# Optimization experiments

Hardware: AMD Instinct MI355X
Metric: run time of the kernel (lower is better)

Reference implementation:

```python
import jax, jax.numpy as jnp
import numpy as np

B, D, C = 512, 512, 100000
U_M, L_M, U_A, L_A = 0.8, 0.45, 110.0, 10.0
LAMBDA_G, SCALE = 35.0, 64.0


def setup_inputs() -> dict:
    key = jax.random.key(0)
    k1, k2, k3, k4 = jax.random.split(key, 4)
    x = jax.random.normal(k1, (B, D), dtype=jnp.float32)
    # magnitudes in [l_a, u_a] as in MagFace
    x_norm = L_A + (U_A - L_A) * jax.random.uniform(k2, (B,), dtype=jnp.float32)
    labels = jax.random.randint(k3, (B,), 0, C, dtype=jnp.int64)
    weight = jax.random.normal(k4, (C, D), dtype=jnp.float32)
    return {"x": x, "x_norm": x_norm, "labels": labels, "weight": weight}


def _l2norm(a, axis=-1, eps=1e-12):
    return a / jnp.maximum(jnp.linalg.norm(a, axis=axis, keepdims=True), eps)


def reference(x, x_norm, labels, weight):
    # adaptive margin per sample, shape [B]
    margin = (U_M - L_M) / (U_A - L_A) * (x_norm - L_A) + L_M

    # cos_theta = normalize(x) @ normalize(W).T  -> [B, C]
    cos_theta = jnp.clip(_l2norm(x) @ _l2norm(weight).T, -1.0, 1.0)

    theta = jnp.arccos(cos_theta)
    valid = labels != -1  # [B]
    safe_labels = jnp.where(valid, labels, 0)
    # add margin at the target class (only for valid labels)
    add = jnp.where(valid, margin, 0.0)  # [B]
    theta = theta.at[jnp.arange(theta.shape[0]), safe_labels].add(add)

    logits = jnp.cos(theta) * SCALE  # [B, C]

    # cross-entropy, ignoring labels == -1
    lse = jax.nn.logsumexp(logits, axis=-1)  # [B]
    tgt = jnp.take_along_axis(logits, safe_labels[:, None], axis=-1)[:, 0]
    nll = jnp.where(valid, lse - tgt, 0.0)
    n_valid = jnp.maximum(jnp.sum(valid.astype(jnp.float32)), 1.0)
    ce = jnp.sum(nll) / n_valid

    # MagFace G-loss
    g_loss = jnp.mean(x_norm / (U_A * U_A) + 1.0 / x_norm)

    return ce + LAMBDA_G * g_loss
```

## Files before the change

kernel.cpp:

```cpp
#include <hip/hip_runtime.h>

typedef unsigned short u16;
typedef unsigned int u32;
typedef float f32x4 __attribute__((ext_vector_type(4)));
typedef short bf16x8 __attribute__((ext_vector_type(8)));

#define U_M 0.8f
#define L_M 0.45f
#define U_A 110.0f
#define L_A 10.0f
#define LAMBDA_G 35.0f
#define SCALEF 64.0f

__device__ __forceinline__ u16 f2bf(float f) {
  u32 u = __builtin_bit_cast(u32, f);
  u32 r = (u + 0x7fffu + ((u >> 16) & 1u)) >> 16;
  return (u16)r;
}

__device__ __forceinline__ u32 cvtpk(float lo, float hi) {
  u32 r;
  asm("v_cvt_pk_bf16_f32 %0, %1, %2" : "=v"(r) : "v"(lo), "v"(hi));
  return r;
}

__global__ void xnorm_kernel(const float* __restrict__ x, u16* __restrict__ xn, int K) {
  int row = blockIdx.x * 4 + (threadIdx.x >> 6);
  int l = threadIdx.x & 63;
  const float4* p = reinterpret_cast<const float4*>(x + (size_t)row * K) + l * 2;
  float4 a = p[0], b = p[1];
  float s = a.x*a.x + a.y*a.y + a.z*a.z + a.w*a.w
          + b.x*b.x + b.y*b.y + b.z*b.z + b.w*b.w;
  #pragma unroll
  for (int m = 32; m >= 1; m >>= 1) s += __shfl_xor(s, m);
  float inv = rsqrtf(fmaxf(s, 1e-24f));
  u32 q0 = (u32)f2bf(a.x*inv) | ((u32)f2bf(a.y*inv) << 16);
  u32 q1 = (u32)f2bf(a.z*inv) | ((u32)f2bf(a.w*inv) << 16);
  u32 q2 = (u32)f2bf(b.x*inv) | ((u32)f2bf(b.y*inv) << 16);
  u32 q3 = (u32)f2bf(b.z*inv) | ((u32)f2bf(b.w*inv) << 16);
  *reinterpret_cast<uint4*>(xn + (size_t)row * K + l * 8) = make_uint4(q0, q1, q2, q3);
}

__global__ void tgt_kernel(const float* __restrict__ x, const float* __restrict__ W,
                           const int* __restrict__ labels, float* __restrict__ tgtcos, int K) {
  int b = blockIdx.x;
  int l = threadIdx.x;
  int lab = labels[b];
  int labc = lab < 0 ? 0 : lab;
  const float4* px = reinterpret_cast<const float4*>(x + (size_t)b * K) + l * 2;
  const float4* pw = reinterpret_cast<const float4*>(W + (size_t)labc * K) + l * 2;
  float4 a0 = px[0], a1 = px[1], w0 = pw[0], w1 = pw[1];
  float dot = a0.x*w0.x + a0.y*w0.y + a0.z*w0.z + a0.w*w0.w
            + a1.x*w1.x + a1.y*w1.y + a1.z*w1.z + a1.w*w1.w;
  float sx = a0.x*a0.x + a0.y*a0.y + a0.z*a0.z + a0.w*a0.w
           + a1.x*a1.x + a1.y*a1.y + a1.z*a1.z + a1.w*a1.w;
  float sw = w0.x*w0.x + w0.y*w0.y + w0.z*w0.z + w0.w*w0.w
           + w1.x*w1.x + w1.y*w1.y + w1.z*w1.z + w1.w*w1.w;
  #pragma unroll
  for (int m = 32; m >= 1; m >>= 1) {
    dot += __shfl_xor(dot, m);
    sx  += __shfl_xor(sx, m);
    sw  += __shfl_xor(sw, m);
  }
  if (l == 0) {
    float cv = dot * rsqrtf(fmaxf(sx, 1e-24f)) * rsqrtf(fmaxf(sw, 1e-24f));
    tgtcos[b] = fminf(fmaxf(cv, -1.f), 1.f);
  }
}

__global__ __launch_bounds__(512, 4) void gemm_wf32(
    const u16* __restrict__ xn, const float* __restrict__ W,
    const int* __restrict__ labels,
    float* __restrict__ partials, int C, int K, int M) {
  __shared__ u16 sA[2][128 * 64];
  __shared__ u16 sB[128 * 64];
  __shared__ float bsum[4][128];
  __shared__ float sIw[128];
  __shared__ int slab[128];

  int nwg = gridDim.x;
  int id = blockIdx.x;
  int q = nwg >> 3, r = nwg & 7;
  int xcd = id & 7, pos = id >> 3;
  int wg = (xcd < r ? xcd * (q + 1) : r * (q + 1) + (xcd - r) * q) + pos;
  const int bm = wg & 3, bn = wg >> 2;

  const int t = threadIdx.x;
  const int l = t & 63, wid = t >> 6;
  const int wm = wid >> 2, wn_ = wid & 3;
  const int n0 = bn * 128;
  if (t < 128) slab[t] = labels[bm * 128 + t];

  const int c4 = t & 15;
  const int rowL = t >> 4;
  const float* wp[4];
  #pragma unroll
  for (int p = 0; p < 4; ++p) {
    int rr = n0 + p * 32 + rowL;
    rr = rr < C ? rr : C - 1;
    wp[p] = W + (size_t)rr * K + c4 * 4;
  }
  float ssq[4] = {0.f, 0.f, 0.f, 0.f};

  const int nkt = K >> 6;
  float4 v[4];

  #pragma unroll
  for (int p = 0; p < 4; ++p) v[p] = *reinterpret_cast<const float4*>(wp[p]);
  #pragma unroll
  for (int i = 0; i < 2; ++i) {
    int L = i * 512 + t;
    int rr = L >> 3;
    int cs = (L & 7) ^ (rr & 7);
    const u16* src = xn + (size_t)(bm * 128 + rr) * K + cs * 8;
    __builtin_amdgcn_global_load_lds(
        (const __attribute__((address_space(1))) void*)src,
        (__attribute__((address_space(3))) void*)(sA[0] + (size_t)(i * 512 + (t & 448)) * 8),
        16, 0, 0);
  }
  #pragma unroll
  for (int p = 0; p < 4; ++p) {
    float4 f = v[p];
    ssq[p] += f.x*f.x + f.y*f.y + f.z*f.z + f.w*f.w;
    int rr = p * 32 + rowL;
    uint2 pk = make_uint2(cvtpk(f.x, f.y), cvtpk(f.z, f.w));
    *reinterpret_cast<uint2*>(sB + rr * 64 + (((c4 >> 1) ^ (rr & 7)) * 8) + (c4 & 1) * 4) = pk;
  }
  __syncthreads();

  f32x4 acc[4][2] = {};
  for (int kt = 0; kt < nkt; ++kt) {
    const bool pf = (kt + 1) < nkt;
    const u16* aCur = sA[kt & 1];

    if (pf) {
      const int k1 = (kt + 1) << 6;
      #pragma unroll
      for (int p = 0; p < 4; ++p) v[p] = *reinterpret_cast<const float4*>(wp[p] + k1);
      u16* aNxt = sA[(kt + 1) & 1];
      #pragma unroll
      for (int i = 0; i < 2; ++i) {
        int L = i * 512 + t;
        int rr = L >> 3;
        int cs = (L & 7) ^ (rr & 7);
        const u16* src = xn + (size_t)(bm * 128 + rr) * K + k1 + cs * 8;
        __builtin_amdgcn_global_load_lds(
            (const __attribute__((address_space(1))) void*)src,
            (__attribute__((address_space(3))) void*)(aNxt + (size_t)(i * 512 + (t & 448)) * 8),
            16, 0, 0);
      }
    }

    #pragma unroll
    for (int ks = 0; ks < 2; ++ks) {
      bf16x8 af[4], bfr[2];
      #pragma unroll
      for (int mi = 0; mi < 4; ++mi) {
        int row = wm * 64 + mi * 16 + (l & 15);
        int ch = ks * 4 + (l >> 4);
        af[mi] = *reinterpret_cast<const bf16x8*>(aCur + row * 64 + ((ch ^ (row & 7)) * 8));
      }
      #pragma unroll
      for (int ni = 0; ni < 2; ++ni) {
        int row = wn_ * 32 + ni * 16 + (l & 15);
        int ch = ks * 4 + (l >> 4);
        bfr[ni] = *reinterpret_cast<const bf16x8*>(sB + row * 64 + ((ch ^ (row & 7)) * 8));
      }
      #pragma unroll
      for (int mi = 0; mi < 4; ++mi)
        #pragma unroll
        for (int ni = 0; ni < 2; ++ni)
          acc[mi][ni] = __builtin_amdgcn_mfma_f32_16x16x32_bf16(af[mi], bfr[ni], acc[mi][ni], 0, 0, 0);
    }

    __syncthreads();

    if (pf) {
      #pragma unroll
      for (int p = 0; p < 4; ++p) {
        float4 f = v[p];
        ssq[p] += f.x*f.x + f.y*f.y + f.z*f.z + f.w*f.w;
        int rr = p * 32 + rowL;
        uint2 pk = make_uint2(cvtpk(f.x, f.y), cvtpk(f.z, f.w));
        *reinterpret_cast<uint2*>(sB + rr * 64 + (((c4 >> 1) ^ (rr & 7)) * 8) + (c4 & 1) * 4) = pk;
      }
    }
    __syncthreads();
  }

  #pragma unroll
  for (int p = 0; p < 4; ++p) {
    float s = ssq[p];
    s += __shfl_xor(s, 1);
    s += __shfl_xor(s, 2);
    s += __shfl_xor(s, 4);
    s += __shfl_xor(s, 8);
    if (c4 == 0) sIw[p * 32 + rowL] = rsqrtf(fmaxf(s, 1e-24f));
  }
  __syncthreads();

  float iw[2]; int colv[2];
  #pragma unroll
  for (int ni = 0; ni < 2; ++ni) {
    int cl = wn_ * 32 + ni * 16 + (l & 15);
    colv[ni] = n0 + cl;
    iw[ni] = sIw[cl];
  }
  #pragma unroll
  for (int mi = 0; mi < 4; ++mi) {
    #pragma unroll
    for (int rg = 0; rg < 4; ++rg) {
      int row_l = wm * 64 + mi * 16 + ((l >> 4) << 2) + rg;
      int labr = slab[row_l];
      float rs = 0.f;
      #pragma unroll
      for (int ni = 0; ni < 2; ++ni) {
        float cv = acc[mi][ni][rg] * iw[ni];
        cv = fminf(fmaxf(cv, -1.f), 1.f);
        float e = __expf(SCALEF * cv - SCALEF);
        bool keep = (colv[ni] < C) && (colv[ni] != labr);
        rs += keep ? e : 0.f;
      }
      rs += __shfl_xor(rs, 1);
      rs += __shfl_xor(rs, 2);
      rs += __shfl_xor(rs, 4);
      rs += __shfl_xor(rs, 8);
      if ((l & 15) == 0) bsum[wn_][row_l] = rs;
    }
  }
  __syncthreads();
  if (t < 128) {
    partials[(size_t)bn * M + bm * 128 + t] =
        (bsum[0][t] + bsum[1][t]) + (bsum[2][t] + bsum[3][t]);
  }
}

__global__ void rowreduce_kernel(const float* __restrict__ partials, float* __restrict__ rowsum,
                                 int NBN, int M) {
  int b = blockIdx.x, t = threadIdx.x;
  float s = 0.f;
  for (int i = t; i < NBN; i += 256) s += partials[(size_t)i * M + b];
  __shared__ float sh[256];
  sh[t] = s; __syncthreads();
  for (int off = 128; off >= 1; off >>= 1) {
    if (t < off) sh[t] += sh[t + off];
    __syncthreads();
  }
  if (t == 0) rowsum[b] = sh[0];
}

__global__ void final_kernel(const float* __restrict__ rowsum, const float* __restrict__ tgtcos,
                             const float* __restrict__ x_norm, const int* __restrict__ labels,
                             float* __restrict__ out, int Bn) {
  int t = threadIdx.x;
  float nll = 0.f, g = 0.f, vld = 0.f;
  if (t < Bn) {
    float a = x_norm[t];
    g = a * (1.0f / (U_A * U_A)) + 1.0f / a;
    int lab = labels[t];
    bool valid = (lab != -1);
    if (valid) {
      float ct = tgtcos[t];
      float margin = ((U_M - L_M) / (U_A - L_A)) * (a - L_A) + L_M;
      float theta = acosf(ct) + margin;
      float tl = SCALEF * cosf(theta);
      float se = rowsum[t] + __expf(tl - SCALEF);
      float lse = SCALEF + logf(se);
      nll = lse - tl;
      vld = 1.f;
    }
  }
  __shared__ float s1[512], s2[512], s3[512];
  s1[t] = nll; s2[t] = g; s3[t] = vld;
  __syncthreads();
  for (int off = 256; off >= 1; off >>= 1) {
    if (t < off) { s1[t] += s1[t + off]; s2[t] += s2[t + off]; s3[t] += s3[t + off]; }
    __syncthreads();
  }
  if (t == 0) {
    float ce = s1[0] / fmaxf(s3[0], 1.f);
    out[0] = ce + LAMBDA_G * (s2[0] / (float)Bn);
  }
}

extern "C" void kernel_launch(void* const* d_in, const int* in_sizes, int n_in,
                              void* d_out, int out_size, void* d_ws, size_t ws_size,
                              hipStream_t stream) {
  const float* x      = (const float*)d_in[0];
  const float* x_norm = (const float*)d_in[1];
  const int*   labels = (const int*)d_in[2];
  const float* W      = (const float*)d_in[3];
  float* out = (float*)d_out;

  const int B = in_sizes[1];
  const int D = in_sizes[0] / B;
  const int C = in_sizes[3] / D;
  const int NBN = (C + 127) / 128;

  char* ws = (char*)d_ws;
  size_t o_xn   = 0;
  size_t o_tgt  = o_xn + (size_t)B * D * 2;
  size_t o_rows = o_tgt + (size_t)B * 4;
  size_t o_part = o_rows + (size_t)B * 4;

  u16*   xn       = (u16*)(ws + o_xn);
  float* tgtcos   = (float*)(ws + o_tgt);
  float* rowsum   = (float*)(ws + o_rows);
  float* partials = (float*)(ws + o_part);

  hipLaunchKernelGGL(xnorm_kernel, dim3(B / 4), dim3(256), 0, stream, x, xn, D);
  hipLaunchKernelGGL(tgt_kernel, dim3(B), dim3(64), 0, stream, x, W, labels, tgtcos, D);
  hipLaunchKernelGGL(gemm_wf32, dim3(NBN * (B / 128)), dim3(512), 0, stream,
                     xn, W, labels, partials, C, D, B);
  hipLaunchKernelGGL(rowreduce_kernel, dim3(B), dim3(256), 0, stream, partials, rowsum, NBN, B);
  hipLaunchKernelGGL(final_kernel, dim3(1), dim3(B), 0, stream, rowsum, tgtcos, x_norm, labels, out, B);
}
```

Before: 124.4 us.

## Use tall 512x128 tiles so each W tile is read and converted once

The GEMM block now covers all 512 batch rows against a 128-class slice, so each W tile is loaded from global memory and converted fp32->bf16 only once instead of four times across four row blocks. Each wave handles 64 rows by 128 columns with a 4x8 MFMA accumulator, and writes its row partial sums directly, dropping the shared-memory cross-wave reduction. The cost is much higher register and LDS use (about 128KB of A double buffer), lower occupancy (launch bounds of 2), a four-times-smaller grid, and reliance on B being exactly 512.

```diff
diff --git a/kernel.cpp b/kernel.cpp
--- a/kernel.cpp
+++ b/kernel.cpp
@@ -68,28 +68,22 @@
   }
 }
 
-__global__ __launch_bounds__(512, 4) void gemm_wf32(
+__global__ __launch_bounds__(512, 2) void gemm_tall(
     const u16* __restrict__ xn, const float* __restrict__ W,
     const int* __restrict__ labels,
     float* __restrict__ partials, int C, int K, int M) {
-  __shared__ u16 sA[2][128 * 64];
+  __shared__ u16 sA[2][512 * 64];
   __shared__ u16 sB[128 * 64];
-  __shared__ float bsum[4][128];
   __shared__ float sIw[128];
-  __shared__ int slab[128];
-
-  int nwg = gridDim.x;
-  int id = blockIdx.x;
-  int q = nwg >> 3, r = nwg & 7;
-  int xcd = id & 7, pos = id >> 3;
-  int wg = (xcd < r ? xcd * (q + 1) : r * (q + 1) + (xcd - r) * q) + pos;
-  const int bm = wg & 3, bn = wg >> 2;
-
+  __shared__ int slab[512];
+
+  const int bn = blockIdx.x;
+  const int n0 = bn * 128;
   const int t = threadIdx.x;
-  const int l = t & 63, wid = t >> 6;
-  const int wm = wid >> 2, wn_ = wid & 3;
-  const int n0 = bn * 128;
-  if (t < 128) slab[t] = labels[bm * 128 + t];
+  const int l = t & 63;
+  const int w = t >> 6;
+
+  slab[t] = labels[t];
 
   const int c4 = t & 15;
   const int rowL = t >> 4;
@@ -108,11 +102,11 @@
   #pragma unroll
   for (int p = 0; p < 4; ++p) v[p] = *reinterpret_cast<const float4*>(wp[p]);
   #pragma unroll
-  for (int i = 0; i < 2; ++i) {
+  for (int i = 0; i < 8; ++i) {
     int L = i * 512 + t;
     int rr = L >> 3;
     int cs = (L & 7) ^ (rr & 7);
-    const u16* src = xn + (size_t)(bm * 128 + rr) * K + cs * 8;
+    const u16* src = xn + (size_t)rr * K + cs * 8;
     __builtin_amdgcn_global_load_lds(
         (const __attribute__((address_space(1))) void*)src,
         (__attribute__((address_space(3))) void*)(sA[0] + (size_t)(i * 512 + (t & 448)) * 8),
@@ -128,7 +122,7 @@
   }
   __syncthreads();
 
-  f32x4 acc[4][2] = {};
+  f32x4 acc[4][8] = {};
   for (int kt = 0; kt < nkt; ++kt) {
     const bool pf = (kt + 1) < nkt;
     const u16* aCur = sA[kt & 1];
@@ -139,11 +133,11 @@
       for (int p = 0; p < 4; ++p) v[p] = *reinterpret_cast<const float4*>(wp[p] + k1);
       u16* aNxt = sA[(kt + 1) & 1];
       #pragma unroll
-      for (int i = 0; i < 2; ++i) {
+      for (int i = 0; i < 8; ++i) {
         int L = i * 512 + t;
         int rr = L >> 3;
         int cs = (L & 7) ^ (rr & 7);
-        const u16* src = xn + (size_t)(bm * 128 + rr) * K + k1 + cs * 8;
+        const u16* src = xn + (size_t)rr * K + k1 + cs * 8;
         __builtin_amdgcn_global_load_lds(
             (const __attribute__((address_space(1))) void*)src,
             (__attribute__((address_space(3))) void*)(aNxt + (size_t)(i * 512 + (t & 448)) * 8),
@@ -153,23 +147,23 @@
 
     #pragma unroll
     for (int ks = 0; ks < 2; ++ks) {
-      bf16x8 af[4], bfr[2];
+      bf16x8 af[4], bfr[8];
       #pragma unroll
       for (int mi = 0; mi < 4; ++mi) {
-        int row = wm * 64 + mi * 16 + (l & 15);
+        int row = w * 64 + mi * 16 + (l & 15);
         int ch = ks * 4 + (l >> 4);
         af[mi] = *reinterpret_cast<const bf16x8*>(aCur + row * 64 + ((ch ^ (row & 7)) * 8));
       }
       #pragma unroll
-      for (int ni = 0; ni < 2; ++ni) {
-        int row = wn_ * 32 + ni * 16 + (l & 15);
+      for (int ni = 0; ni < 8; ++ni) {
+        int row = ni * 16 + (l & 15);
         int ch = ks * 4 + (l >> 4);
         bfr[ni] = *reinterpret_cast<const bf16x8*>(sB + row * 64 + ((ch ^ (row & 7)) * 8));
       }
       #pragma unroll
       for (int mi = 0; mi < 4; ++mi)
         #pragma unroll
-        for (int ni = 0; ni < 2; ++ni)
+        for (int ni = 0; ni < 8; ++ni)
           acc[mi][ni] = __builtin_amdgcn_mfma_f32_16x16x32_bf16(af[mi], bfr[ni], acc[mi][ni], 0, 0, 0);
     }
 
@@ -199,10 +193,10 @@
   }
   __syncthreads();
 
-  float iw[2]; int colv[2];
-  #pragma unroll
-  for (int ni = 0; ni < 2; ++ni) {
-    int cl = wn_ * 32 + ni * 16 + (l & 15);
+  float iw[8]; int colv[8];
+  #pragma unroll
+  for (int ni = 0; ni < 8; ++ni) {
+    int cl = ni * 16 + (l & 15);
     colv[ni] = n0 + cl;
     iw[ni] = sIw[cl];
   }
@@ -210,11 +204,11 @@
   for (int mi = 0; mi < 4; ++mi) {
     #pragma unroll
     for (int rg = 0; rg < 4; ++rg) {
-      int row_l = wm * 64 + mi * 16 + ((l >> 4) << 2) + rg;
+      int row_l = w * 64 + mi * 16 + ((l >> 4) << 2) + rg;
       int labr = slab[row_l];
       float rs = 0.f;
       #pragma unroll
-      for (int ni = 0; ni < 2; ++ni) {
+      for (int ni = 0; ni < 8; ++ni) {
         float cv = acc[mi][ni][rg] * iw[ni];
         cv = fminf(fmaxf(cv, -1.f), 1.f);
         float e = __expf(SCALEF * cv - SCALEF);
@@ -225,13 +219,8 @@
       rs += __shfl_xor(rs, 2);
       rs += __shfl_xor(rs, 4);
       rs += __shfl_xor(rs, 8);
-      if ((l & 15) == 0) bsum[wn_][row_l] = rs;
-    }
-  }
-  __syncthreads();
-  if (t < 128) {
-    partials[(size_t)bn * M + bm * 128 + t] =
-        (bsum[0][t] + bsum[1][t]) + (bsum[2][t] + bsum[3][t]);
+      if ((l & 15) == 0) partials[(size_t)bn * M + row_l] = rs;
+    }
   }
 }
 
@@ -310,7 +299,7 @@
 
   hipLaunchKernelGGL(xnorm_kernel, dim3(B / 4), dim3(256), 0, stream, x, xn, D);
   hipLaunchKernelGGL(tgt_kernel, dim3(B), dim3(64), 0, stream, x, W, labels, tgtcos, D);
-  hipLaunchKernelGGL(gemm_wf32, dim3(NBN * (B / 128)), dim3(512), 0, stream,
+  hipLaunchKernelGGL(gemm_tall, dim3(NBN), dim3(512), 0, stream,
                      xn, W, labels, partials, C, D, B);
   hipLaunchKernelGGL(rowreduce_kernel, dim3(B), dim3(256), 0, stream, partials, rowsum, NBN, B);
   hipLaunchKernelGGL(final_kernel, dim3(1), dim3(B), 0, stream, rowsum, tgtcos, x_norm, labels, out, B);
```

After: 138.5 us. 1.11x slower.
